# Kernel tuning notes

Measured on AMD Instinct MI355X. Metric: run time of the kernel, lower is better.

Reference implementation:

```python
import jax, jax.numpy as jnp
import numpy as np

EPS = 1e-5
KEY_DIM = 32
V_DIM = 128  # att_ratio * key_dim
HEADS = 8


def bn2d(x, g, b):
    # BatchNorm2d, training-mode batch statistics: per-channel over (B, H, W)
    m = x.mean(axis=(0, 2, 3), keepdims=True)
    v = x.var(axis=(0, 2, 3), keepdims=True)
    xh = (x - m) * jax.lax.rsqrt(v + EPS)
    return xh * g[None, :, None, None] + b[None, :, None, None]


def conv1x1(x, w):
    # [B,Cin,H,W] x [Cout,Cin] -> [B,Cout,H,W]
    return jnp.einsum('bchw,oc->bohw', x, w)


def setup_inputs() -> dict:
    key = jax.random.key(0)
    ks = jax.random.split(key, 6)
    B, C, H, W = 8, 384, 32, 32
    s = 0.02
    return {
        'x': jax.random.normal(ks[0], (B, C, H, W), jnp.float32),
        'w_qkv': jax.random.normal(ks[1], (1536, 384), jnp.float32) * s,
        'g_qkv': jnp.ones((1536,), jnp.float32),
        'b_qkv': jnp.zeros((1536,), jnp.float32),
        'w_merge': jax.random.normal(ks[2], (384, 1024), jnp.float32) * s,
        'g_merge': jnp.ones((384,), jnp.float32),
        'b_merge': jnp.zeros((384,), jnp.float32),
        'w_fc1': jax.random.normal(ks[3], (768, 384), jnp.float32) * s,
        'g_fc1': jnp.ones((768,), jnp.float32),
        'b_fc1': jnp.zeros((768,), jnp.float32),
        'w_fc2': jax.random.normal(ks[4], (384, 768), jnp.float32) * s,
        'g_fc2': jnp.ones((384,), jnp.float32),
        'b_fc2': jnp.zeros((384,), jnp.float32),
    }


def reference(x, w_qkv, g_qkv, b_qkv, w_merge, g_merge, b_merge,
              w_fc1, g_fc1, b_fc1, w_fc2, g_fc2, b_fc2):
    B, C, H, W = x.shape
    N = H * W
    scale = KEY_DIM ** -0.5

    # ---- Attention block (conv path) ----
    qkv = bn2d(conv1x1(x, w_qkv), g_qkv, b_qkv)            # [B,1536,H,W]
    qkv = qkv.reshape(B, HEADS, KEY_DIM + KEY_DIM + V_DIM, N)
    q = qkv[:, :, :KEY_DIM]                                 # [B,h,dq,N]
    k = qkv[:, :, KEY_DIM:2 * KEY_DIM]                      # [B,h,dk,N]
    v = qkv[:, :, 2 * KEY_DIM:]                             # [B,h,dv,N]
    att = jnp.einsum('bhdn,bhdm->bhnm', q, k) * scale       # [B,h,N,N]
    att = jax.nn.softmax(att, axis=-1)
    o = jnp.einsum('bhnm,bhdm->bhdn', att, v)               # [B,h,dv,N]
    o = o.reshape(B, HEADS * V_DIM, H, W)                   # [B,1024,H,W]
    o = jax.nn.gelu(o, approximate=False)                   # merge.act
    o = bn2d(conv1x1(o, w_merge), g_merge, b_merge)         # [B,384,H,W]
    x = x + o                                               # residual

    # ---- ConvMlp block ----
    h = bn2d(conv1x1(x, w_fc1), g_fc1, b_fc1)               # [B,768,H,W]
    h = jax.nn.gelu(h, approximate=False)
    h = bn2d(conv1x1(h, w_fc2), g_fc2, b_fc2)               # [B,384,H,W]
    return x + h
```

## Files before the change

kernel.cpp:

```cpp
#include <hip/hip_runtime.h>
#include <hip/hip_bf16.h>
#include <math.h>


#define ROWS 8192
#define NPIX 1024

typedef __attribute__((ext_vector_type(8))) short short8;
typedef __attribute__((ext_vector_type(4))) float f32x4;

__device__ __forceinline__ float gelu_exact(float v) {
    return 0.5f * v * (1.0f + erff(v * 0.70710678118654752f));
}
__device__ __forceinline__ short f2bf(float f) {
    unsigned u = __float_as_uint(f);
    unsigned r = (u + 0x7fffu + ((u >> 16) & 1u)) >> 16;
    return (short)r;
}
__device__ __forceinline__ unsigned long long pack4bf(float a, float b, float c, float d) {
    return  (unsigned long long)(unsigned short)f2bf(a)
         | ((unsigned long long)(unsigned short)f2bf(b) << 16)
         | ((unsigned long long)(unsigned short)f2bf(c) << 32)
         | ((unsigned long long)(unsigned short)f2bf(d) << 48);
}

__global__ __launch_bounds__(256) void cast_bf(const float* __restrict__ s,
                                               short* __restrict__ d, int n8) {
    int t = blockIdx.x * 256 + threadIdx.x;
    if (t >= n8) return;
    float4 a = *(const float4*)&s[(size_t)t * 8];
    float4 b = *(const float4*)&s[(size_t)t * 8 + 4];
    short8 o;
    o[0]=f2bf(a.x); o[1]=f2bf(a.y); o[2]=f2bf(a.z); o[3]=f2bf(a.w);
    o[4]=f2bf(b.x); o[5]=f2bf(b.y); o[6]=f2bf(b.z); o[7]=f2bf(b.w);
    *(short8*)&d[(size_t)t * 8] = o;
}

__global__ __launch_bounds__(256) void x_transpose(
    const float* __restrict__ x, short* __restrict__ x_bf, float* __restrict__ x_tf)
{
    __shared__ float ls[64][65];
    const int b = blockIdx.z, c0 = blockIdx.y * 64, n0 = blockIdx.x * 64;
    const int rl = threadIdx.x >> 6, ll = threadIdx.x & 63;
    #pragma unroll
    for (int it = 0; it < 16; ++it) {
        int c = rl + it * 4;
        ls[c][ll] = x[((size_t)b * 384 + c0 + c) * NPIX + n0 + ll];
    }
    __syncthreads();
    #pragma unroll
    for (int it = 0; it < 16; ++it) {
        int n = rl + it * 4;
        float v = ls[ll][n];
        size_t row = (size_t)b * NPIX + n0 + n;
        x_tf[row * 384 + c0 + ll] = v;
        x_bf[row * 384 + c0 + ll] = f2bf(v);
    }
}

#define LDK 72
__global__ __launch_bounds__(256) void gemm_bf16(
    const short* __restrict__ A, const short* __restrict__ Wt,
    float* __restrict__ D, float* __restrict__ sums, int O, int K)
{
    __shared__ short a_s[128 * LDK];
    __shared__ short w_s[128 * LDK];
    const int tid = threadIdx.x;
    const int wave = tid >> 6, lane = tid & 63;
    const int l16 = lane & 15, lhi = lane >> 4;
    const int m0 = blockIdx.x * 128, o0 = blockIdx.y * 128;
    const int wm = (wave & 1) * 64, wo = (wave >> 1) * 64;

    f32x4 acc[4][4];
    #pragma unroll
    for (int i = 0; i < 4; ++i)
        #pragma unroll
        for (int j = 0; j < 4; ++j) acc[i][j] = (f32x4){0.f, 0.f, 0.f, 0.f};

    for (int k0 = 0; k0 < K; k0 += 64) {
        #pragma unroll
        for (int it = 0; it < 4; ++it) {
            int idx = tid + it * 256;
            int r = idx >> 3, ch = idx & 7;
            *(float4*)&a_s[r * LDK + ch * 8] =
                *(const float4*)&A[(size_t)(m0 + r) * K + k0 + ch * 8];
            *(float4*)&w_s[r * LDK + ch * 8] =
                *(const float4*)&Wt[(size_t)(o0 + r) * K + k0 + ch * 8];
        }
        __syncthreads();
        #pragma unroll
        for (int kb = 0; kb < 2; ++kb) {
            short8 af[4], wf[4];
            #pragma unroll
            for (int i = 0; i < 4; ++i)
                af[i] = *(const short8*)&a_s[(wm + i * 16 + l16) * LDK + kb * 32 + lhi * 8];
            #pragma unroll
            for (int j = 0; j < 4; ++j)
                wf[j] = *(const short8*)&w_s[(wo + j * 16 + l16) * LDK + kb * 32 + lhi * 8];
            #pragma unroll
            for (int i = 0; i < 4; ++i)
                #pragma unroll
                for (int j = 0; j < 4; ++j)
                    acc[i][j] = __builtin_amdgcn_mfma_f32_16x16x32_bf16(af[i], wf[j], acc[i][j], 0, 0, 0);
        }
        __syncthreads();
    }

    #pragma unroll
    for (int i = 0; i < 4; ++i) {
        #pragma unroll
        for (int r = 0; r < 4; ++r) {
            size_t row = (size_t)(m0 + wm + i * 16 + lhi * 4 + r);
            #pragma unroll
            for (int j = 0; j < 4; ++j)
                D[row * O + o0 + wo + j * 16 + l16] = acc[i][j][r];
        }
    }
    #pragma unroll
    for (int j = 0; j < 4; ++j) {
        float s1 = 0.f, s2 = 0.f;
        #pragma unroll
        for (int i = 0; i < 4; ++i)
            #pragma unroll
            for (int r = 0; r < 4; ++r) { float v = acc[i][j][r]; s1 += v; s2 += v * v; }
        s1 += __shfl_xor(s1, 16); s1 += __shfl_xor(s1, 32);
        s2 += __shfl_xor(s2, 16); s2 += __shfl_xor(s2, 32);
        if (lhi == 0) {
            int col = o0 + wo + j * 16 + l16;
            atomicAdd(&sums[col * 2], s1);
            atomicAdd(&sums[col * 2 + 1], s2);
        }
    }
}

__global__ __launch_bounds__(256) void bn_finalize(
    const float* __restrict__ sums, const float* __restrict__ gamma,
    const float* __restrict__ beta, float* __restrict__ st, int O)
{
    int ch = blockIdx.x * 256 + threadIdx.x;
    if (ch >= O) return;
    float s = sums[ch * 2], ss = sums[ch * 2 + 1];
    float mean = s * (1.0f / 8192.0f);
    float var = ss * (1.0f / 8192.0f) - mean * mean;
    float sc = gamma[ch] * rsqrtf(var + 1e-5f);
    st[ch * 2] = sc;
    st[ch * 2 + 1] = beta[ch] - mean * sc;
}

__global__ __launch_bounds__(256) void qkv_post(
    const float* __restrict__ raw, const float* __restrict__ st, short* __restrict__ qk)
{
    int t = blockIdx.x * 256 + threadIdx.x;
    int row = t >> 7, g = t & 127;
    int c = g * 4;
    int h = c >> 6, r = c & 63;
    int ch = h * 192 + r;
    float4 v = *(const float4*)&raw[(size_t)row * 1536 + ch];
    float4 sa = *(const float4*)&st[ch * 2];
    float4 sb = *(const float4*)&st[ch * 2 + 4];
    float o0 = v.x * sa.x + sa.y, o1 = v.y * sa.z + sa.w;
    float o2 = v.z * sb.x + sb.y, o3 = v.w * sb.z + sb.w;
    if (r < 32) {
        const float invsq = 0.17677669529663687f;
        o0 *= invsq; o1 *= invsq; o2 *= invsq; o3 *= invsq;
    }
    *(unsigned long long*)&qk[(size_t)row * 512 + c] = pack4bf(o0, o1, o2, o3);
}

__global__ __launch_bounds__(256) void v_transpose(
    const float* __restrict__ raw, const float* __restrict__ st, short* __restrict__ vt)
{
    __shared__ short ls[64][72];
    const int bh = blockIdx.z, b = bh >> 3, h = bh & 7;
    const int dv0 = blockIdx.y * 64, n0 = blockIdx.x * 64;
    const int rl = threadIdx.x >> 6, ll = threadIdx.x & 63;
    const int ch = h * 192 + 64 + dv0 + ll;
    const float sc = st[ch * 2], sh = st[ch * 2 + 1];
    #pragma unroll
    for (int it = 0; it < 16; ++it) {
        int n = rl + it * 4;
        float v = raw[((size_t)b * NPIX + n0 + n) * 1536 + ch] * sc + sh;
        ls[n][ll] = f2bf(v);
    }
    __syncthreads();
    #pragma unroll
    for (int it = 0; it < 16; ++it) {
        int dv = rl + it * 4;
        vt[((size_t)bh * 128 + dv0 + dv) * NPIX + n0 + ll] = ls[ll][dv];
    }
}

__global__ __launch_bounds__(256) void attn_kernel(
    const short* __restrict__ qk, const short* __restrict__ vt, short* __restrict__ outp)
{
    __shared__ short k_s[64 * 40];
    __shared__ short vt_s[128 * 72];
    __shared__ short p_s[4 * 32 * 72];

    const int qt = blockIdx.x, h = blockIdx.y, b = blockIdx.z;
    const int q0 = qt * 128;
    const int tid = threadIdx.x;
    const int wave = tid >> 6, lane = tid & 63;
    const int l16 = lane & 15, lhi = lane >> 4;
    const int wq = wave * 32;
    short* pw = &p_s[wave * 32 * 72];

    short8 qf[2];
    #pragma unroll
    for (int fq = 0; fq < 2; ++fq) {
        size_t row = (size_t)b * NPIX + q0 + wq + fq * 16 + l16;
        qf[fq] = *(const short8*)&qk[row * 512 + h * 64 + lhi * 8];
    }

    f32x4 acc[2][8];
    #pragma unroll
    for (int i = 0; i < 2; ++i)
        #pragma unroll
        for (int j = 0; j < 8; ++j) acc[i][j] = (f32x4){0.f, 0.f, 0.f, 0.f};
    float m_run[2][4], l_run[2][4];
    #pragma unroll
    for (int i = 0; i < 2; ++i)
        #pragma unroll
        for (int r = 0; r < 4; ++r) { m_run[i][r] = -1e30f; l_run[i][r] = 0.f; }

    for (int mt = 0; mt < 16; ++mt) {
        const int m0 = mt * 64;
        {
            int r = tid >> 2, ch = tid & 3;
            size_t row = (size_t)b * NPIX + m0 + r;
            *(float4*)&k_s[r * 40 + ch * 8] =
                *(const float4*)&qk[row * 512 + h * 64 + 32 + ch * 8];
        }
        #pragma unroll
        for (int it = 0; it < 4; ++it) {
            int idx = tid + it * 256;
            int r = idx >> 3, ch = idx & 7;
            *(float4*)&vt_s[r * 72 + ch * 8] =
                *(const float4*)&vt[((size_t)(b * 8 + h) * 128 + r) * NPIX + m0 + ch * 8];
        }
        __syncthreads();

        f32x4 s[2][4];
        #pragma unroll
        for (int i = 0; i < 2; ++i)
            #pragma unroll
            for (int j = 0; j < 4; ++j) s[i][j] = (f32x4){0.f, 0.f, 0.f, 0.f};
        #pragma unroll
        for (int fm = 0; fm < 4; ++fm) {
            short8 kf = *(const short8*)&k_s[(fm * 16 + l16) * 40 + lhi * 8];
            #pragma unroll
            for (int fq = 0; fq < 2; ++fq)
                s[fq][fm] = __builtin_amdgcn_mfma_f32_16x16x32_bf16(qf[fq], kf, s[fq][fm], 0, 0, 0);
        }

        #pragma unroll
        for (int fq = 0; fq < 2; ++fq) {
            #pragma unroll
            for (int rr = 0; rr < 4; ++rr) {
                float mx = fmaxf(fmaxf(s[fq][0][rr], s[fq][1][rr]),
                                 fmaxf(s[fq][2][rr], s[fq][3][rr]));
                #pragma unroll
                for (int msk = 1; msk < 16; msk <<= 1) mx = fmaxf(mx, __shfl_xor(mx, msk));
                float mo = m_run[fq][rr];
                float mn = fmaxf(mo, mx);
                float f = __expf(mo - mn);
                m_run[fq][rr] = mn;
                int qrow = fq * 16 + lhi * 4 + rr;
                float rsum = 0.f;
                #pragma unroll
                for (int fm = 0; fm < 4; ++fm) {
                    float p = __expf(s[fq][fm][rr] - mn);
                    rsum += p;
                    pw[qrow * 72 + fm * 16 + l16] = f2bf(p);
                }
                #pragma unroll
                for (int msk = 1; msk < 16; msk <<= 1) rsum += __shfl_xor(rsum, msk);
                l_run[fq][rr] = l_run[fq][rr] * f + rsum;
                #pragma unroll
                for (int fdv = 0; fdv < 8; ++fdv) acc[fq][fdv][rr] *= f;
            }
        }
        __syncthreads();

        #pragma unroll
        for (int kc = 0; kc < 2; ++kc) {
            short8 pf[2];
            pf[0] = *(const short8*)&pw[(l16) * 72 + kc * 32 + lhi * 8];
            pf[1] = *(const short8*)&pw[(16 + l16) * 72 + kc * 32 + lhi * 8];
            #pragma unroll
            for (int fdv = 0; fdv < 8; ++fdv) {
                short8 vf = *(const short8*)&vt_s[(fdv * 16 + l16) * 72 + kc * 32 + lhi * 8];
                #pragma unroll
                for (int fq = 0; fq < 2; ++fq)
                    acc[fq][fdv] = __builtin_amdgcn_mfma_f32_16x16x32_bf16(pf[fq], vf, acc[fq][fdv], 0, 0, 0);
            }
        }
        __syncthreads();
    }

    #pragma unroll
    for (int fq = 0; fq < 2; ++fq) {
        #pragma unroll
        for (int rr = 0; rr < 4; ++rr) {
            float inv = 1.0f / l_run[fq][rr];
            size_t row = (size_t)b * NPIX + q0 + wq + fq * 16 + lhi * 4 + rr;
            #pragma unroll
            for (int fdv = 0; fdv < 8; ++fdv) {
                float o = acc[fq][fdv][rr] * inv;
                outp[row * 1024 + h * 128 + fdv * 16 + l16] = f2bf(gelu_exact(o));
            }
        }
    }
}

__global__ __launch_bounds__(256) void x2_kernel(
    const float* __restrict__ raw, const float* __restrict__ st,
    const float* __restrict__ xtf, float* __restrict__ x2f, short* __restrict__ x2bf)
{
    int t = blockIdx.x * 256 + threadIdx.x;
    int row = t / 96, c = (t % 96) * 4;
    size_t idx = (size_t)row * 384 + c;
    float4 v = *(const float4*)&raw[idx];
    float4 xr = *(const float4*)&xtf[idx];
    float4 sa = *(const float4*)&st[c * 2];
    float4 sb = *(const float4*)&st[c * 2 + 4];
    float o0 = xr.x + v.x * sa.x + sa.y;
    float o1 = xr.y + v.y * sa.z + sa.w;
    float o2 = xr.z + v.z * sb.x + sb.y;
    float o3 = xr.w + v.w * sb.z + sb.w;
    *(float4*)&x2f[idx] = make_float4(o0, o1, o2, o3);
    *(unsigned long long*)&x2bf[idx] = pack4bf(o0, o1, o2, o3);
}

__global__ __launch_bounds__(256) void h_kernel(
    const float* __restrict__ raw, const float* __restrict__ st, short* __restrict__ hbf)
{
    int t = blockIdx.x * 256 + threadIdx.x;
    int row = t / 192, c = (t % 192) * 4;
    size_t idx = (size_t)row * 768 + c;
    float4 v = *(const float4*)&raw[idx];
    float4 sa = *(const float4*)&st[c * 2];
    float4 sb = *(const float4*)&st[c * 2 + 4];
    float o0 = gelu_exact(v.x * sa.x + sa.y);
    float o1 = gelu_exact(v.y * sa.z + sa.w);
    float o2 = gelu_exact(v.z * sb.x + sb.y);
    float o3 = gelu_exact(v.w * sb.z + sb.w);
    *(unsigned long long*)&hbf[idx] = pack4bf(o0, o1, o2, o3);
}

__global__ __launch_bounds__(256) void final_tr(
    const float* __restrict__ raw, const float* __restrict__ st,
    const float* __restrict__ x2f, float* __restrict__ out)
{
    __shared__ float ls[64][65];
    const int b = blockIdx.z, c0 = blockIdx.y * 64, n0 = blockIdx.x * 64;
    const int rl = threadIdx.x >> 6, ll = threadIdx.x & 63;
    const int c = c0 + ll;
    const float sc = st[c * 2], sh = st[c * 2 + 1];
    #pragma unroll
    for (int it = 0; it < 16; ++it) {
        int n = rl + it * 4;
        size_t idx = ((size_t)b * NPIX + n0 + n) * 384 + c;
        ls[n][ll] = x2f[idx] + raw[idx] * sc + sh;
    }
    __syncthreads();
    #pragma unroll
    for (int it = 0; it < 16; ++it) {
        int cr = rl + it * 4;
        out[((size_t)b * 384 + c0 + cr) * NPIX + n0 + ll] = ls[ll][cr];
    }
}

extern "C" void kernel_launch(void* const* d_in, const int* in_sizes, int n_in,
                              void* d_out, int out_size, void* d_ws, size_t ws_size,
                              hipStream_t stream)
{
    const float* x       = (const float*)d_in[0];
    const float* w_qkv   = (const float*)d_in[1];
    const float* g_qkv   = (const float*)d_in[2];
    const float* b_qkv   = (const float*)d_in[3];
    const float* w_merge = (const float*)d_in[4];
    const float* g_merge = (const float*)d_in[5];
    const float* b_merge = (const float*)d_in[6];
    const float* w_fc1   = (const float*)d_in[7];
    const float* g_fc1   = (const float*)d_in[8];
    const float* b_fc1   = (const float*)d_in[9];
    const float* w_fc2   = (const float*)d_in[10];
    const float* g_fc2   = (const float*)d_in[11];
    const float* b_fc2   = (const float*)d_in[12];
    float* out = (float*)d_out;

    char* ws = (char*)d_ws;
    short* wq_bf   = (short*)(ws + 0);
    short* wm_bf   = (short*)(ws + 1179648);
    short* wf1_bf  = (short*)(ws + 1966080);
    short* wf2_bf  = (short*)(ws + 2555904);
    short* x_bf    = (short*)(ws + 3145728);
    float* x_tf    = (float*)(ws + 9437184);
    float* qkv_raw = (float*)(ws + 22020096);
    short* qk_bf   = (short*)(ws + 72351744);
    short* vt      = (short*)(ws + 80740352);
    short* attn_bf = (short*)(ws + 22020096);
    float* fc1_raw = (float*)(ws + 38797312);
    float* fc2_raw = (float*)(ws + 22020096);
    short* h_bf    = (short*)(ws + 80740352);
    float* merge_raw = (float*)(ws + 97517568);
    short* x2_bf   = (short*)(ws + 110100480);
    float* x2_f    = (float*)(ws + 116391936);
    float* sums    = (float*)(ws + 128974848);
    float* stats   = (float*)(ws + 128999424);

    float* sums_qkv = sums;
    float* sums_mg  = sums + 1536 * 2;
    float* sums_f1  = sums + (1536 + 384) * 2;
    float* sums_f2  = sums + (1536 + 384 + 768) * 2;
    float* st_qkv = stats;
    float* st_mg  = stats + 1536 * 2;
    float* st_f1  = stats + (1536 + 384) * 2;
    float* st_f2  = stats + (1536 + 384 + 768) * 2;

    hipMemsetAsync(sums, 0, 3072 * 2 * sizeof(float), stream);

    cast_bf<<<288, 256, 0, stream>>>(w_qkv, wq_bf, 1536 * 384 / 8);
    cast_bf<<<192, 256, 0, stream>>>(w_merge, wm_bf, 384 * 1024 / 8);
    cast_bf<<<144, 256, 0, stream>>>(w_fc1, wf1_bf, 768 * 384 / 8);
    cast_bf<<<144, 256, 0, stream>>>(w_fc2, wf2_bf, 384 * 768 / 8);

    x_transpose<<<dim3(16, 6, 8), 256, 0, stream>>>(x, x_bf, x_tf);

    gemm_bf16<<<dim3(64, 12), 256, 0, stream>>>(x_bf, wq_bf, qkv_raw, sums_qkv, 1536, 384);
    bn_finalize<<<6, 256, 0, stream>>>(sums_qkv, g_qkv, b_qkv, st_qkv, 1536);
    qkv_post<<<4096, 256, 0, stream>>>(qkv_raw, st_qkv, qk_bf);
    v_transpose<<<dim3(16, 2, 64), 256, 0, stream>>>(qkv_raw, st_qkv, vt);

    attn_kernel<<<dim3(8, 8, 8), 256, 0, stream>>>(qk_bf, vt, attn_bf);

    gemm_bf16<<<dim3(64, 3), 256, 0, stream>>>(attn_bf, wm_bf, merge_raw, sums_mg, 384, 1024);
    bn_finalize<<<2, 256, 0, stream>>>(sums_mg, g_merge, b_merge, st_mg, 384);
    x2_kernel<<<3072, 256, 0, stream>>>(merge_raw, st_mg, x_tf, x2_f, x2_bf);

    gemm_bf16<<<dim3(64, 6), 256, 0, stream>>>(x2_bf, wf1_bf, fc1_raw, sums_f1, 768, 384);
    bn_finalize<<<3, 256, 0, stream>>>(sums_f1, g_fc1, b_fc1, st_f1, 768);
    h_kernel<<<6144, 256, 0, stream>>>(fc1_raw, st_f1, h_bf);

    gemm_bf16<<<dim3(64, 3), 256, 0, stream>>>(h_bf, wf2_bf, fc2_raw, sums_f2, 384, 768);
    bn_finalize<<<2, 256, 0, stream>>>(sums_f2, g_fc2, b_fc2, st_f2, 384);
    final_tr<<<dim3(16, 6, 8), 256, 0, stream>>>(fc2_raw, st_f2, x2_f, out);
}
```

Measured before the change: 356.1 us.

## Fuse BN finalize into consumers, merge casts, restructure attention to single-wave blocks

```diff
diff --git a/kernel.cpp b/kernel.cpp
--- a/kernel.cpp
+++ b/kernel.cpp
@@ -3,11 +3,10 @@
 #include <math.h>
 
 
-#define ROWS 8192
 #define NPIX 1024
-
 typedef __attribute__((ext_vector_type(8))) short short8;
 typedef __attribute__((ext_vector_type(4))) float f32x4;
+typedef unsigned long long ull;
 
 __device__ __forceinline__ float gelu_exact(float v) {
     return 0.5f * v * (1.0f + erff(v * 0.70710678118654752f));
@@ -17,23 +16,36 @@
     unsigned r = (u + 0x7fffu + ((u >> 16) & 1u)) >> 16;
     return (short)r;
 }
-__device__ __forceinline__ unsigned long long pack4bf(float a, float b, float c, float d) {
-    return  (unsigned long long)(unsigned short)f2bf(a)
-         | ((unsigned long long)(unsigned short)f2bf(b) << 16)
-         | ((unsigned long long)(unsigned short)f2bf(c) << 32)
-         | ((unsigned long long)(unsigned short)f2bf(d) << 48);
-}
-
-__global__ __launch_bounds__(256) void cast_bf(const float* __restrict__ s,
-                                               short* __restrict__ d, int n8) {
+__device__ __forceinline__ ull pack4bf(float a, float b, float c, float d) {
+    return  (ull)(unsigned short)f2bf(a)
+         | ((ull)(unsigned short)f2bf(b) << 16)
+         | ((ull)(unsigned short)f2bf(c) << 32)
+         | ((ull)(unsigned short)f2bf(d) << 48);
+}
+__device__ __forceinline__ void bn_sc(float s, float ss, float g, float bt,
+                                      float& sc, float& sh) {
+    float mean = s * (1.0f / 8192.0f);
+    float var  = ss * (1.0f / 8192.0f) - mean * mean;
+    sc = g * rsqrtf(var + 1e-5f);
+    sh = bt - mean * sc;
+}
+
+__global__ __launch_bounds__(256) void cast4(
+    const float* __restrict__ s0, const float* __restrict__ s1,
+    const float* __restrict__ s2, const float* __restrict__ s3,
+    short* __restrict__ d0, short* __restrict__ d1,
+    short* __restrict__ d2, short* __restrict__ d3)
+{
     int t = blockIdx.x * 256 + threadIdx.x;
-    if (t >= n8) return;
-    float4 a = *(const float4*)&s[(size_t)t * 8];
-    float4 b = *(const float4*)&s[(size_t)t * 8 + 4];
-    short8 o;
-    o[0]=f2bf(a.x); o[1]=f2bf(a.y); o[2]=f2bf(a.z); o[3]=f2bf(a.w);
-    o[4]=f2bf(b.x); o[5]=f2bf(b.y); o[6]=f2bf(b.z); o[7]=f2bf(b.w);
-    *(short8*)&d[(size_t)t * 8] = o;
+    const float* s; short* d; int off;
+    if (t < 73728)       { s = s0; d = d0; off = t; }
+    else if (t < 122880) { s = s1; d = d1; off = t - 73728; }
+    else if (t < 159744) { s = s2; d = d2; off = t - 122880; }
+    else                 { s = s3; d = d3; off = t - 159744; }
+    float4 a = *(const float4*)&s[(size_t)off * 8];
+    float4 b = *(const float4*)&s[(size_t)off * 8 + 4];
+    *(ull*)&d[(size_t)off * 8]     = pack4bf(a.x, a.y, a.z, a.w);
+    *(ull*)&d[(size_t)off * 8 + 4] = pack4bf(b.x, b.y, b.z, b.w);
 }
 
 __global__ __launch_bounds__(256) void x_transpose(
@@ -58,47 +70,53 @@
     }
 }
 
-#define LDK 72
+template<int NAF>
 __global__ __launch_bounds__(256) void gemm_bf16(
     const short* __restrict__ A, const short* __restrict__ Wt,
     float* __restrict__ D, float* __restrict__ sums, int O, int K)
 {
-    __shared__ short a_s[128 * LDK];
-    __shared__ short w_s[128 * LDK];
+    constexpr int BM = NAF * 32;
+    __shared__ short a_s[BM * 72];
+    __shared__ short w_s[128 * 72];
     const int tid = threadIdx.x;
     const int wave = tid >> 6, lane = tid & 63;
     const int l16 = lane & 15, lhi = lane >> 4;
-    const int m0 = blockIdx.x * 128, o0 = blockIdx.y * 128;
-    const int wm = (wave & 1) * 64, wo = (wave >> 1) * 64;
-
-    f32x4 acc[4][4];
-    #pragma unroll
-    for (int i = 0; i < 4; ++i)
+    const int m0 = blockIdx.x * BM, o0 = blockIdx.y * 128;
+    const int wm = (wave & 1) * (BM / 2), wo = (wave >> 1) * 64;
+
+    f32x4 acc[NAF][4];
+    #pragma unroll
+    for (int i = 0; i < NAF; ++i)
         #pragma unroll
         for (int j = 0; j < 4; ++j) acc[i][j] = (f32x4){0.f, 0.f, 0.f, 0.f};
 
     for (int k0 = 0; k0 < K; k0 += 64) {
+        #pragma unroll
+        for (int it = 0; it < NAF; ++it) {
+            int idx = tid + it * 256;
+            int r = idx >> 3, ch = idx & 7;
+            *(float4*)&a_s[r * 72 + ch * 8] =
+                *(const float4*)&A[(size_t)(m0 + r) * K + k0 + ch * 8];
+        }
         #pragma unroll
         for (int it = 0; it < 4; ++it) {
             int idx = tid + it * 256;
             int r = idx >> 3, ch = idx & 7;
-            *(float4*)&a_s[r * LDK + ch * 8] =
-                *(const float4*)&A[(size_t)(m0 + r) * K + k0 + ch * 8];
-            *(float4*)&w_s[r * LDK + ch * 8] =
+            *(float4*)&w_s[r * 72 + ch * 8] =
                 *(const float4*)&Wt[(size_t)(o0 + r) * K + k0 + ch * 8];
         }
         __syncthreads();
         #pragma unroll
         for (int kb = 0; kb < 2; ++kb) {
-            short8 af[4], wf[4];
-            #pragma unroll
-            for (int i = 0; i < 4; ++i)
-                af[i] = *(const short8*)&a_s[(wm + i * 16 + l16) * LDK + kb * 32 + lhi * 8];
+            short8 af[NAF], wf[4];
+            #pragma unroll
+            for (int i = 0; i < NAF; ++i)
+                af[i] = *(const short8*)&a_s[(wm + i * 16 + l16) * 72 + kb * 32 + lhi * 8];
             #pragma unroll
             for (int j = 0; j < 4; ++j)
-                wf[j] = *(const short8*)&w_s[(wo + j * 16 + l16) * LDK + kb * 32 + lhi * 8];
-            #pragma unroll
-            for (int i = 0; i < 4; ++i)
+                wf[j] = *(const short8*)&w_s[(wo + j * 16 + l16) * 72 + kb * 32 + lhi * 8];
+            #pragma unroll
+            for (int i = 0; i < NAF; ++i)
                 #pragma unroll
                 for (int j = 0; j < 4; ++j)
                     acc[i][j] = __builtin_amdgcn_mfma_f32_16x16x32_bf16(af[i], wf[j], acc[i][j], 0, 0, 0);
@@ -107,7 +125,7 @@
     }
 
     #pragma unroll
-    for (int i = 0; i < 4; ++i) {
+    for (int i = 0; i < NAF; ++i) {
         #pragma unroll
         for (int r = 0; r < 4; ++r) {
             size_t row = (size_t)(m0 + wm + i * 16 + lhi * 4 + r);
@@ -120,7 +138,7 @@
     for (int j = 0; j < 4; ++j) {
         float s1 = 0.f, s2 = 0.f;
         #pragma unroll
-        for (int i = 0; i < 4; ++i)
+        for (int i = 0; i < NAF; ++i)
             #pragma unroll
             for (int r = 0; r < 4; ++r) { float v = acc[i][j][r]; s1 += v; s2 += v * v; }
         s1 += __shfl_xor(s1, 16); s1 += __shfl_xor(s1, 32);
@@ -133,84 +151,92 @@
     }
 }
 
-__global__ __launch_bounds__(256) void bn_finalize(
-    const float* __restrict__ sums, const float* __restrict__ gamma,
-    const float* __restrict__ beta, float* __restrict__ st, int O)
-{
-    int ch = blockIdx.x * 256 + threadIdx.x;
-    if (ch >= O) return;
-    float s = sums[ch * 2], ss = sums[ch * 2 + 1];
-    float mean = s * (1.0f / 8192.0f);
-    float var = ss * (1.0f / 8192.0f) - mean * mean;
-    float sc = gamma[ch] * rsqrtf(var + 1e-5f);
-    st[ch * 2] = sc;
-    st[ch * 2 + 1] = beta[ch] - mean * sc;
-}
-
-__global__ __launch_bounds__(256) void qkv_post(
-    const float* __restrict__ raw, const float* __restrict__ st, short* __restrict__ qk)
-{
-    int t = blockIdx.x * 256 + threadIdx.x;
-    int row = t >> 7, g = t & 127;
-    int c = g * 4;
-    int h = c >> 6, r = c & 63;
-    int ch = h * 192 + r;
-    float4 v = *(const float4*)&raw[(size_t)row * 1536 + ch];
-    float4 sa = *(const float4*)&st[ch * 2];
-    float4 sb = *(const float4*)&st[ch * 2 + 4];
-    float o0 = v.x * sa.x + sa.y, o1 = v.y * sa.z + sa.w;
-    float o2 = v.z * sb.x + sb.y, o3 = v.w * sb.z + sb.w;
-    if (r < 32) {
-        const float invsq = 0.17677669529663687f;
-        o0 *= invsq; o1 *= invsq; o2 *= invsq; o3 *= invsq;
-    }
-    *(unsigned long long*)&qk[(size_t)row * 512 + c] = pack4bf(o0, o1, o2, o3);
-}
-
-__global__ __launch_bounds__(256) void v_transpose(
-    const float* __restrict__ raw, const float* __restrict__ st, short* __restrict__ vt)
-{
-    __shared__ short ls[64][72];
-    const int bh = blockIdx.z, b = bh >> 3, h = bh & 7;
-    const int dv0 = blockIdx.y * 64, n0 = blockIdx.x * 64;
-    const int rl = threadIdx.x >> 6, ll = threadIdx.x & 63;
-    const int ch = h * 192 + 64 + dv0 + ll;
-    const float sc = st[ch * 2], sh = st[ch * 2 + 1];
-    #pragma unroll
-    for (int it = 0; it < 16; ++it) {
-        int n = rl + it * 4;
-        float v = raw[((size_t)b * NPIX + n0 + n) * 1536 + ch] * sc + sh;
-        ls[n][ll] = f2bf(v);
-    }
-    __syncthreads();
-    #pragma unroll
-    for (int it = 0; it < 16; ++it) {
-        int dv = rl + it * 4;
-        vt[((size_t)bh * 128 + dv0 + dv) * NPIX + n0 + ll] = ls[ll][dv];
-    }
-}
-
-__global__ __launch_bounds__(256) void attn_kernel(
+__global__ __launch_bounds__(256) void qkv_post_vt(
+    const float* __restrict__ raw, const float* __restrict__ sums,
+    const float* __restrict__ gamma, const float* __restrict__ beta,
+    short* __restrict__ qko, short* __restrict__ vto)
+{
+    __shared__ short ls[64][136];
+    const int b = blockIdx.z, hp = blockIdx.y, n0 = blockIdx.x * 64;
+    const int tid = threadIdx.x;
+    const int r = tid >> 2, cg = tid & 3;
+    const size_t rowbase = (size_t)(b * NPIX + n0 + r) * 1536;
+    const float qs = 0.17677669529663687f * 1.4426950408889634f;
+
+    {
+        int hh = 2 * hp + (cg >> 1);
+        int chb = hh * 192 + (cg & 1) * 32;
+        bool isq = (cg & 1) == 0;
+        size_t orow = (size_t)(b * NPIX + n0 + r) * 512 + hp * 128 + cg * 32;
+        #pragma unroll
+        for (int cc = 0; cc < 8; ++cc) {
+            int ch = chb + cc * 4;
+            float4 v  = *(const float4*)&raw[rowbase + ch];
+            float4 s1 = *(const float4*)&sums[ch * 2];
+            float4 s2 = *(const float4*)&sums[ch * 2 + 4];
+            float4 gg = *(const float4*)&gamma[ch];
+            float4 bb = *(const float4*)&beta[ch];
+            float sc, sh, o[4];
+            bn_sc(s1.x, s1.y, gg.x, bb.x, sc, sh); o[0] = v.x * sc + sh;
+            bn_sc(s1.z, s1.w, gg.y, bb.y, sc, sh); o[1] = v.y * sc + sh;
+            bn_sc(s2.x, s2.y, gg.z, bb.z, sc, sh); o[2] = v.z * sc + sh;
+            bn_sc(s2.z, s2.w, gg.w, bb.w, sc, sh); o[3] = v.w * sc + sh;
+            if (isq) { o[0] *= qs; o[1] *= qs; o[2] *= qs; o[3] *= qs; }
+            *(ull*)&qko[orow + cc * 4] = pack4bf(o[0], o[1], o[2], o[3]);
+        }
+    }
+    #pragma unroll
+    for (int hv = 0; hv < 2; ++hv) {
+        int h = 2 * hp + hv;
+        __syncthreads();
+        #pragma unroll
+        for (int cc = 0; cc < 8; ++cc) {
+            int ch = h * 192 + 64 + cg * 32 + cc * 4;
+            float4 v  = *(const float4*)&raw[rowbase + ch];
+            float4 s1 = *(const float4*)&sums[ch * 2];
+            float4 s2 = *(const float4*)&sums[ch * 2 + 4];
+            float4 gg = *(const float4*)&gamma[ch];
+            float4 bb = *(const float4*)&beta[ch];
+            float sc, sh, o[4];
+            bn_sc(s1.x, s1.y, gg.x, bb.x, sc, sh); o[0] = v.x * sc + sh;
+            bn_sc(s1.z, s1.w, gg.y, bb.y, sc, sh); o[1] = v.y * sc + sh;
+            bn_sc(s2.x, s2.y, gg.z, bb.z, sc, sh); o[2] = v.z * sc + sh;
+            bn_sc(s2.z, s2.w, gg.w, bb.w, sc, sh); o[3] = v.w * sc + sh;
+            *(ull*)&ls[r][cg * 32 + cc * 4] = pack4bf(o[0], o[1], o[2], o[3]);
+        }
+        __syncthreads();
+        int dv = tid >> 1, nh = tid & 1;
+        size_t obase = ((size_t)(b * 8 + h) * 128 + dv) * NPIX + n0 + nh * 32;
+        #pragma unroll
+        for (int j = 0; j < 8; ++j) {
+            int n = nh * 32 + j * 4;
+            ull u =  (ull)(unsigned short)ls[n][dv]
+                  | ((ull)(unsigned short)ls[n + 1][dv] << 16)
+                  | ((ull)(unsigned short)ls[n + 2][dv] << 32)
+                  | ((ull)(unsigned short)ls[n + 3][dv] << 48);
+            *(ull*)&vto[obase + j * 4] = u;
+        }
+    }
+}
+
+__global__ __launch_bounds__(64) void attn_kernel(
     const short* __restrict__ qk, const short* __restrict__ vt, short* __restrict__ outp)
 {
-    __shared__ short k_s[64 * 40];
-    __shared__ short vt_s[128 * 72];
-    __shared__ short p_s[4 * 32 * 72];
-
-    const int qt = blockIdx.x, h = blockIdx.y, b = blockIdx.z;
-    const int q0 = qt * 128;
-    const int tid = threadIdx.x;
-    const int wave = tid >> 6, lane = tid & 63;
+    __shared__ short pw[32 * 72];
+    const int id0 = blockIdx.x;
+    const int swz = (id0 & 7) * 256 + (id0 >> 3);
+    const int qt = swz & 31, bh = swz >> 5;
+    const int h = bh & 7, b = bh >> 3;
+    const int q0 = qt * 32;
+    const int lane = threadIdx.x;
     const int l16 = lane & 15, lhi = lane >> 4;
-    const int wq = wave * 32;
-    short* pw = &p_s[wave * 32 * 72];
+
+    const short* qkb = qk + (size_t)b * NPIX * 512 + h * 64;
+    const short* vb  = vt + (size_t)bh * 128 * NPIX;
 
     short8 qf[2];
-    #pragma unroll
-    for (int fq = 0; fq < 2; ++fq) {
-        size_t row = (size_t)b * NPIX + q0 + wq + fq * 16 + l16;
-        qf[fq] = *(const short8*)&qk[row * 512 + h * 64 + lhi * 8];
-    }
+    qf[0] = *(const short8*)&qkb[(size_t)(q0 + l16) * 512 + lhi * 8];
+    qf[1] = *(const short8*)&qkb[(size_t)(q0 + 16 + l16) * 512 + lhi * 8];
 
     f32x4 acc[2][8];
     #pragma unroll
@@ -225,20 +251,10 @@
 
     for (int mt = 0; mt < 16; ++mt) {
         const int m0 = mt * 64;
-        {
-            int r = tid >> 2, ch = tid & 3;
-            size_t row = (size_t)b * NPIX + m0 + r;
-            *(float4*)&k_s[r * 40 + ch * 8] =
-                *(const float4*)&qk[row * 512 + h * 64 + 32 + ch * 8];
-        }
-        #pragma unroll
-        for (int it = 0; it < 4; ++it) {
-            int idx = tid + it * 256;
-            int r = idx >> 3, ch = idx & 7;
-            *(float4*)&vt_s[r * 72 + ch * 8] =
-                *(const float4*)&vt[((size_t)(b * 8 + h) * 128 + r) * NPIX + m0 + ch * 8];
-        }
-        __syncthreads();
+        short8 kf[4];
+        #pragma unroll
+        for (int fm = 0; fm < 4; ++fm)
+            kf[fm] = *(const short8*)&qkb[(size_t)(m0 + fm * 16 + l16) * 512 + 32 + lhi * 8];
 
         f32x4 s[2][4];
         #pragma unroll
@@ -246,117 +262,141 @@
             #pragma unroll
             for (int j = 0; j < 4; ++j) s[i][j] = (f32x4){0.f, 0.f, 0.f, 0.f};
         #pragma unroll
-        for (int fm = 0; fm < 4; ++fm) {
-            short8 kf = *(const short8*)&k_s[(fm * 16 + l16) * 40 + lhi * 8];
+        for (int fm = 0; fm < 4; ++fm)
             #pragma unroll
             for (int fq = 0; fq < 2; ++fq)
-                s[fq][fm] = __builtin_amdgcn_mfma_f32_16x16x32_bf16(qf[fq], kf, s[fq][fm], 0, 0, 0);
-        }
-
-        #pragma unroll
-        for (int fq = 0; fq < 2; ++fq) {
+                s[fq][fm] = __builtin_amdgcn_mfma_f32_16x16x32_bf16(qf[fq], kf[fm], s[fq][fm], 0, 0, 0);
+
+        float mx[2][4];
+        bool need = false;
+        #pragma unroll
+        for (int fq = 0; fq < 2; ++fq)
             #pragma unroll
             for (int rr = 0; rr < 4; ++rr) {
-                float mx = fmaxf(fmaxf(s[fq][0][rr], s[fq][1][rr]),
+                float m1 = fmaxf(fmaxf(s[fq][0][rr], s[fq][1][rr]),
                                  fmaxf(s[fq][2][rr], s[fq][3][rr]));
+                m1 = fmaxf(m1, __shfl_xor(m1, 1));
+                m1 = fmaxf(m1, __shfl_xor(m1, 2));
+                m1 = fmaxf(m1, __shfl_xor(m1, 4));
+                m1 = fmaxf(m1, __shfl_xor(m1, 8));
+                mx[fq][rr] = m1;
+                need |= (m1 > m_run[fq][rr] + 11.0f);
+            }
+        if (__any(need)) {
+            #pragma unroll
+            for (int fq = 0; fq < 2; ++fq)
                 #pragma unroll
-                for (int msk = 1; msk < 16; msk <<= 1) mx = fmaxf(mx, __shfl_xor(mx, msk));
-                float mo = m_run[fq][rr];
-                float mn = fmaxf(mo, mx);
-                float f = __expf(mo - mn);
-                m_run[fq][rr] = mn;
-                int qrow = fq * 16 + lhi * 4 + rr;
+                for (int rr = 0; rr < 4; ++rr) {
+                    float mn = fmaxf(m_run[fq][rr], mx[fq][rr]);
+                    float f = exp2f(m_run[fq][rr] - mn);
+                    m_run[fq][rr] = mn;
+                    l_run[fq][rr] *= f;
+                    #pragma unroll
+                    for (int fdv = 0; fdv < 8; ++fdv) acc[fq][fdv][rr] *= f;
+                }
+        }
+        #pragma unroll
+        for (int fq = 0; fq < 2; ++fq)
+            #pragma unroll
+            for (int rr = 0; rr < 4; ++rr) {
+                float mr = m_run[fq][rr];
                 float rsum = 0.f;
                 #pragma unroll
                 for (int fm = 0; fm < 4; ++fm) {
-                    float p = __expf(s[fq][fm][rr] - mn);
+                    float p = exp2f(s[fq][fm][rr] - mr);
                     rsum += p;
-                    pw[qrow * 72 + fm * 16 + l16] = f2bf(p);
+                    pw[(fq * 16 + lhi * 4 + rr) * 72 + fm * 16 + l16] = f2bf(p);
                 }
-                #pragma unroll
-                for (int msk = 1; msk < 16; msk <<= 1) rsum += __shfl_xor(rsum, msk);
-                l_run[fq][rr] = l_run[fq][rr] * f + rsum;
-                #pragma unroll
-                for (int fdv = 0; fdv < 8; ++fdv) acc[fq][fdv][rr] *= f;
+                rsum += __shfl_xor(rsum, 1);
+                rsum += __shfl_xor(rsum, 2);
+                rsum += __shfl_xor(rsum, 4);
+                rsum += __shfl_xor(rsum, 8);
+                l_run[fq][rr] += rsum;
             }
-        }
-        __syncthreads();
+        asm volatile("s_waitcnt lgkmcnt(0)" ::: "memory");
 
         #pragma unroll
         for (int kc = 0; kc < 2; ++kc) {
-            short8 pf[2];
-            pf[0] = *(const short8*)&pw[(l16) * 72 + kc * 32 + lhi * 8];
-            pf[1] = *(const short8*)&pw[(16 + l16) * 72 + kc * 32 + lhi * 8];
+            short8 pf0 = *(const short8*)&pw[(l16) * 72 + kc * 32 + lhi * 8];
+            short8 pf1 = *(const short8*)&pw[(16 + l16) * 72 + kc * 32 + lhi * 8];
             #pragma unroll
             for (int fdv = 0; fdv < 8; ++fdv) {
-                short8 vf = *(const short8*)&vt_s[(fdv * 16 + l16) * 72 + kc * 32 + lhi * 8];
-                #pragma unroll
-                for (int fq = 0; fq < 2; ++fq)
-                    acc[fq][fdv] = __builtin_amdgcn_mfma_f32_16x16x32_bf16(pf[fq], vf, acc[fq][fdv], 0, 0, 0);
+                short8 vf = *(const short8*)&vb[(size_t)(fdv * 16 + l16) * NPIX + m0 + kc * 32 + lhi * 8];
+                acc[0][fdv] = __builtin_amdgcn_mfma_f32_16x16x32_bf16(pf0, vf, acc[0][fdv], 0, 0, 0);
+                acc[1][fdv] = __builtin_amdgcn_mfma_f32_16x16x32_bf16(pf1, vf, acc[1][fdv], 0, 0, 0);
             }
         }
-        __syncthreads();
-    }
-
-    #pragma unroll
-    for (int fq = 0; fq < 2; ++fq) {
+    }
+
+    #pragma unroll
+    for (int fq = 0; fq < 2; ++fq)
         #pragma unroll
         for (int rr = 0; rr < 4; ++rr) {
             float inv = 1.0f / l_run[fq][rr];
-            size_t row = (size_t)b * NPIX + q0 + wq + fq * 16 + lhi * 4 + rr;
+            size_t row = (size_t)b * NPIX + q0 + fq * 16 + lhi * 4 + rr;
             #pragma unroll
             for (int fdv = 0; fdv < 8; ++fdv) {
                 float o = acc[fq][fdv][rr] * inv;
                 outp[row * 1024 + h * 128 + fdv * 16 + l16] = f2bf(gelu_exact(o));
             }
         }
-    }
 }
 
 __global__ __launch_bounds__(256) void x2_kernel(
-    const float* __restrict__ raw, const float* __restrict__ st,
+    const float* __restrict__ raw, const float* __restrict__ sums,
+    const float* __restrict__ gamma, const float* __restrict__ beta,
     const float* __restrict__ xtf, float* __restrict__ x2f, short* __restrict__ x2bf)
 {
     int t = blockIdx.x * 256 + threadIdx.x;
     int row = t / 96, c = (t % 96) * 4;
     size_t idx = (size_t)row * 384 + c;
-    float4 v = *(const float4*)&raw[idx];
+    float4 v  = *(const float4*)&raw[idx];
     float4 xr = *(const float4*)&xtf[idx];
-    float4 sa = *(const float4*)&st[c * 2];
-    float4 sb = *(const float4*)&st[c * 2 + 4];
-    float o0 = xr.x + v.x * sa.x + sa.y;
-    float o1 = xr.y + v.y * sa.z + sa.w;
-    float o2 = xr.z + v.z * sb.x + sb.y;
-    float o3 = xr.w + v.w * sb.z + sb.w;
+    float4 s1 = *(const float4*)&sums[c * 2];
+    float4 s2 = *(const float4*)&sums[c * 2 + 4];
+    float4 gg = *(const float4*)&gamma[c];
+    float4 bb = *(const float4*)&beta[c];
+    float sc, sh;
+    bn_sc(s1.x, s1.y, gg.x, bb.x, sc, sh); float o0 = xr.x + v.x * sc + sh;
+    bn_sc(s1.z, s1.w, gg.y, bb.y, sc, sh); float o1 = xr.y + v.y * sc + sh;
+    bn_sc(s2.x, s2.y, gg.z, bb.z, sc, sh); float o2 = xr.z + v.z * sc + sh;
+    bn_sc(s2.z, s2.w, gg.w, bb.w, sc, sh); float o3 = xr.w + v.w * sc + sh;
     *(float4*)&x2f[idx] = make_float4(o0, o1, o2, o3);
-    *(unsigned long long*)&x2bf[idx] = pack4bf(o0, o1, o2, o3);
+    *(ull*)&x2bf[idx] = pack4bf(o0, o1, o2, o3);
 }
 
 __global__ __launch_bounds__(256) void h_kernel(
-    const float* __restrict__ raw, const float* __restrict__ st, short* __restrict__ hbf)
+    const float* __restrict__ raw, const float* __restrict__ sums,
+    const float* __restrict__ gamma, const float* __restrict__ beta,
+    short* __restrict__ hbf)
 {
     int t = blockIdx.x * 256 + threadIdx.x;
     int row = t / 192, c = (t % 192) * 4;
     size_t idx = (size_t)row * 768 + c;
-    float4 v = *(const float4*)&raw[idx];
-    float4 sa = *(const float4*)&st[c * 2];
-    float4 sb = *(const float4*)&st[c * 2 + 4];
-    float o0 = gelu_exact(v.x * sa.x + sa.y);
-    float o1 = gelu_exact(v.y * sa.z + sa.w);
-    float o2 = gelu_exact(v.z * sb.x + sb.y);
-    float o3 = gelu_exact(v.w * sb.z + sb.w);
-    *(unsigned long long*)&hbf[idx] = pack4bf(o0, o1, o2, o3);
+    float4 v  = *(const float4*)&raw[idx];
+    float4 s1 = *(const float4*)&sums[c * 2];
+    float4 s2 = *(const float4*)&sums[c * 2 + 4];
+    float4 gg = *(const float4*)&gamma[c];
+    float4 bb = *(const float4*)&beta[c];
+    float sc, sh;
+    bn_sc(s1.x, s1.y, gg.x, bb.x, sc, sh); float o0 = gelu_exact(v.x * sc + sh);
+    bn_sc(s1.z, s1.w, gg.y, bb.y, sc, sh); float o1 = gelu_exact(v.y * sc + sh);
+    bn_sc(s2.x, s2.y, gg.z, bb.z, sc, sh); float o2 = gelu_exact(v.z * sc + sh);
+    bn_sc(s2.z, s2.w, gg.w, bb.w, sc, sh); float o3 = gelu_exact(v.w * sc + sh);
+    *(ull*)&hbf[idx] = pack4bf(o0, o1, o2, o3);
 }
 
 __global__ __launch_bounds__(256) void final_tr(
-    const float* __restrict__ raw, const float* __restrict__ st,
+    const float* __restrict__ raw, const float* __restrict__ sums,
+    const float* __restrict__ gamma, const float* __restrict__ beta,
     const float* __restrict__ x2f, float* __restrict__ out)
 {
     __shared__ float ls[64][65];
     const int b = blockIdx.z, c0 = blockIdx.y * 64, n0 = blockIdx.x * 64;
     const int rl = threadIdx.x >> 6, ll = threadIdx.x & 63;
     const int c = c0 + ll;
-    const float sc = st[c * 2], sh = st[c * 2 + 1];
+    float sc, sh;
+    bn_sc(sums[c * 2], sums[c * 2 + 1], gamma[c], beta[c], sc, sh);
     #pragma unroll
     for (int it = 0; it < 16; ++it) {
         int n = rl + it * 4;
@@ -408,42 +448,29 @@
     short* x2_bf   = (short*)(ws + 110100480);
     float* x2_f    = (float*)(ws + 116391936);
     float* sums    = (float*)(ws + 128974848);
-    float* stats   = (float*)(ws + 128999424);
 
     float* sums_qkv = sums;
     float* sums_mg  = sums + 1536 * 2;
     float* sums_f1  = sums + (1536 + 384) * 2;
     float* sums_f2  = sums + (1536 + 384 + 768) * 2;
-    float* st_qkv = stats;
-    float* st_mg  = stats + 1536 * 2;
-    float* st_f1  = stats + (1536 + 384) * 2;
-    float* st_f2  = stats + (1536 + 384 + 768) * 2;
 
     hipMemsetAsync(sums, 0, 3072 * 2 * sizeof(float), stream);
 
-    cast_bf<<<288, 256, 0, stream>>>(w_qkv, wq_bf, 1536 * 384 / 8);
-    cast_bf<<<192, 256, 0, stream>>>(w_merge, wm_bf, 384 * 1024 / 8);
-    cast_bf<<<144, 256, 0, stream>>>(w_fc1, wf1_bf, 768 * 384 / 8);
-    cast_bf<<<144, 256, 0, stream>>>(w_fc2, wf2_bf, 384 * 768 / 8);
-
+    cast4<<<768, 256, 0, stream>>>(w_qkv, w_merge, w_fc1, w_fc2,
+                                   wq_bf, wm_bf, wf1_bf, wf2_bf);
     x_transpose<<<dim3(16, 6, 8), 256, 0, stream>>>(x, x_bf, x_tf);
 
-    gemm_bf16<<<dim3(64, 12), 256, 0, stream>>>(x_bf, wq_bf, qkv_raw, sums_qkv, 1536, 384);
-    bn_finalize<<<6, 256, 0, stream>>>(sums_qkv, g_qkv, b_qkv, st_qkv, 1536);
-    qkv_post<<<4096, 256, 0, stream>>>(qkv_raw, st_qkv, qk_bf);
-    v_transpose<<<dim3(16, 2, 64), 256, 0, stream>>>(qkv_raw, st_qkv, vt);
-
-    attn_kernel<<<dim3(8, 8, 8), 256, 0, stream>>>(qk_bf, vt, attn_bf);
-
-    gemm_bf16<<<dim3(64, 3), 256, 0, stream>>>(attn_bf, wm_bf, merge_raw, sums_mg, 384, 1024);
-    bn_finalize<<<2, 256, 0, stream>>>(sums_mg, g_merge, b_merge, st_mg, 384);
-    x2_kernel<<<3072, 256, 0, stream>>>(merge_raw, st_mg, x_tf, x2_f, x2_bf);
-
-    gemm_bf16<<<dim3(64, 6), 256, 0, stream>>>(x2_bf, wf1_bf, fc1_raw, sums_f1, 768, 384);
-    bn_finalize<<<3, 256, 0, stream>>>(sums_f1, g_fc1, b_fc1, st_f1, 768);
-    h_kernel<<<6144, 256, 0, stream>>>(fc1_raw, st_f1, h_bf);
-
-    gemm_bf16<<<dim3(64, 3), 256, 0, stream>>>(h_bf, wf2_bf, fc2_raw, sums_f2, 384, 768);
-    bn_finalize<<<2, 256, 0, stream>>>(sums_f2, g_fc2, b_fc2, st_f2, 384);
-    final_tr<<<dim3(16, 6, 8), 256, 0, stream>>>(fc2_raw, st_f2, x2_f, out);
-}
+    gemm_bf16<4><<<dim3(64, 12), 256, 0, stream>>>(x_bf, wq_bf, qkv_raw, sums_qkv, 1536, 384);
+    qkv_post_vt<<<dim3(16, 4, 8), 256, 0, stream>>>(qkv_raw, sums_qkv, g_qkv, b_qkv, qk_bf, vt);
+
+    attn_kernel<<<2048, 64, 0, stream>>>(qk_bf, vt, attn_bf);
+
+    gemm_bf16<2><<<dim3(128, 3), 256, 0, stream>>>(attn_bf, wm_bf, merge_raw, sums_mg, 384, 1024);
+    x2_kernel<<<3072, 256, 0, stream>>>(merge_raw, sums_mg, g_merge, b_merge, x_tf, x2_f, x2_bf);
+
+    gemm_bf16<4><<<dim3(64, 6), 256, 0, stream>>>(x2_bf, wf1_bf, fc1_raw, sums_f1, 768, 384);
+    h_kernel<<<6144, 256, 0, stream>>>(fc1_raw, sums_f1, g_fc1, b_fc1, h_bf);
+
+    gemm_bf16<2><<<dim3(128, 3), 256, 0, stream>>>(h_bf, wf2_bf, fc2_raw, sums_f2, 384, 768);
+    final_tr<<<dim3(16, 6, 8), 256, 0, stream>>>(fc2_raw, sums_f2, g_fc2, b_fc2, x2_f, out);
+}
```

Result: slower. 397.8 us (+11.7%).
